# Kernel tuning notes

Measured on AMD Instinct MI355X. Metric: run time of the kernel, lower is better.

The kernel has to match this reference:

```python
import jax, jax.numpy as jnp
import numpy as np

# ---------- constants ----------
EPS = 1e-5
_rng = np.random.default_rng(0)
_P = _rng.normal(size=(8, 3))
_P /= np.linalg.norm(_P, axis=1, keepdims=True)

def _y2_np(p):
    x, y, z = p[:, 0], p[:, 1], p[:, 2]
    return np.stack([x * y, y * z, 3 * z * z - 1, x * z, x * x - y * y], axis=-1)

_A2 = np.linalg.pinv(_y2_np(_P)).astype(np.float32)  # [5,8]
P_C = jnp.asarray(_P.astype(np.float32))
A2_C = jnp.asarray(_A2)
NORM_CONST = np.float32(1.0 / np.sqrt(20.0))  # avg_num_neighbors ** -0.5
# res update (buffer zeros, not learnable): sigmoid(0)=0.5
_U = 0.5
C_OLD = np.float32(1.0 / np.sqrt(_U * _U + 1.0))
C_NEW = np.float32(_U * C_OLD)


def _y2(p):  # real l=2 monomial basis on unit vectors
    x, y, z = p[..., 0], p[..., 1], p[..., 2]
    return jnp.stack([x * y, y * z, 3.0 * z * z - 1.0, x * z, x * x - y * y], axis=-1)


def _frame(v):  # [E,3] -> R [E,3,3] with R @ v_hat = z
    n = v / jnp.linalg.norm(v, axis=-1, keepdims=True)
    z = jnp.array([0.0, 0.0, 1.0], v.dtype)
    xa = jnp.array([1.0, 0.0, 0.0], v.dtype)
    a = jnp.where(jnp.abs(n[:, 2:3]) < 0.99, z, xa)
    e1 = jnp.cross(a, n)
    e1 = e1 / jnp.linalg.norm(e1, axis=-1, keepdims=True)
    e2 = jnp.cross(n, e1)
    return jnp.stack([e1, e2, n], axis=1)


def _wigner_d2(R):  # [E,3,3] -> D2 [E,5,5] via sample-point fit
    pts = jnp.einsum('pj,eij->epi', P_C, R)  # R @ p_k, [E,8,3]
    M = _y2(pts)  # [E,8,5] = Y_P @ D^T
    Dt = jnp.einsum('ap,epb->eab', A2_C, M)  # [E,5,5]
    return jnp.swapaxes(Dt, 1, 2)


def _sln(x, w0, b0, w1, w2):  # separable equivariant layernorm, 32x0e+16x1e+8x2e
    s = x[:, :32]
    v1 = x[:, 32:80].reshape(-1, 16, 3)
    v2 = x[:, 80:120].reshape(-1, 8, 5)
    mu = jnp.mean(s, axis=-1, keepdims=True)
    var = jnp.mean((s - mu) ** 2, axis=-1, keepdims=True)
    s = (s - mu) * jax.lax.rsqrt(var + EPS) * w0 + b0
    var1 = jnp.mean(v1 ** 2, axis=(1, 2))  # degree-balanced component variance
    var2 = jnp.mean(v2 ** 2, axis=(1, 2))
    inv = jax.lax.rsqrt(0.5 * (var1 + var2) + EPS)[:, None, None]
    v1 = v1 * inv * w1[None, :, None]
    v2 = v2 * inv * w2[None, :, None]
    return jnp.concatenate([s, v1.reshape(-1, 48), v2.reshape(-1, 40)], axis=-1)


def _ir_linear(x, W0, b0, W1, W2):  # irreps-wise linear 32x0e+16x1e+8x2e -> same
    s = x[:, :32] @ (W0 / np.sqrt(32.0)) + b0
    v1 = jnp.einsum('eui,uv->evi', x[:, 32:80].reshape(-1, 16, 3), W1) / np.sqrt(16.0)
    v2 = jnp.einsum('eui,uv->evi', x[:, 80:120].reshape(-1, 8, 5), W2) / np.sqrt(8.0)
    return jnp.concatenate([s, v1.reshape(-1, 48), v2.reshape(-1, 40)], axis=-1)


def _so2(x_cat, R, D2f, D2b, w):  # SO2 linear with per-edge dynamic weights
    E = x_cat.shape[0]
    w0 = w[:, :8960].reshape(E, 112, 80)
    w1r = w[:, 8960:10112].reshape(E, 48, 24)
    w1i = w[:, 10112:11264].reshape(E, 48, 24)
    w2r = w[:, 11264:11392].reshape(E, 16, 8)
    w2i = w[:, 11392:11520].reshape(E, 16, 8)
    # split concatenated [in + hidden] blocks
    s = jnp.concatenate([x_cat[:, :32], x_cat[:, 120:152]], axis=-1)  # [E,64]
    v1 = jnp.concatenate([x_cat[:, 32:80].reshape(E, 16, 3),
                          x_cat[:, 152:200].reshape(E, 16, 3)], axis=1)  # [E,32,3]
    v2 = jnp.concatenate([x_cat[:, 80:120].reshape(E, 8, 5),
                          x_cat[:, 200:240].reshape(E, 16 // 2, 5)], axis=1)  # [E,16,5]
    # rotate into edge-aligned frame
    v1 = jnp.einsum('eij,euj->eui', R, v1)
    v2 = jnp.einsum('eij,euj->eui', D2f, v2)
    in0 = jnp.concatenate([s, v1[:, :, 1], v2[:, :, 2]], axis=-1)   # m=0, [E,112]
    inn1 = jnp.concatenate([v1[:, :, 0], v2[:, :, 1]], axis=-1)     # m=-1, [E,48]
    inp1 = jnp.concatenate([v1[:, :, 2], v2[:, :, 3]], axis=-1)     # m=+1
    inn2 = v2[:, :, 0]  # m=-2
    inp2 = v2[:, :, 4]  # m=+2
    out0 = jnp.einsum('ei,eio->eo', in0, w0) / np.sqrt(112.0)
    op1 = (jnp.einsum('ei,eio->eo', inp1, w1r) - jnp.einsum('ei,eio->eo', inn1, w1i)) / np.sqrt(48.0)
    on1 = (jnp.einsum('ei,eio->eo', inn1, w1r) + jnp.einsum('ei,eio->eo', inp1, w1i)) / np.sqrt(48.0)
    op2 = (jnp.einsum('ei,eio->eo', inp2, w2r) - jnp.einsum('ei,eio->eo', inn2, w2i)) / np.sqrt(16.0)
    on2 = (jnp.einsum('ei,eio->eo', inn2, w2r) + jnp.einsum('ei,eio->eo', inp2, w2i)) / np.sqrt(16.0)
    s_out = out0[:, :56]
    y1 = jnp.stack([on1[:, :16], out0[:, 56:72], op1[:, :16]], axis=-1)  # [E,16,3]
    y2o = jnp.stack([on2, on1[:, 16:24], out0[:, 72:80], op1[:, 16:24], op2], axis=-1)  # [E,8,5]
    # rotate back
    y1 = jnp.einsum('eij,euj->eui', jnp.swapaxes(R, 1, 2), y1)
    y2o = jnp.einsum('eij,euj->eui', D2b, y2o)
    return jnp.concatenate([s_out, y1.reshape(E, 48), y2o.reshape(E, 40)], axis=-1)  # [E,144]


def _gate(m):  # 32x0e scalars | 24x0e gates | 16x1e+8x2e gated
    s = jax.nn.silu(m[:, :32])
    g = jax.nn.sigmoid(m[:, 32:56])
    v1 = m[:, 56:104].reshape(-1, 16, 3) * g[:, :16, None]
    v2 = m[:, 104:144].reshape(-1, 8, 5) * g[:, 16:24, None]
    return jnp.concatenate([s, v1.reshape(-1, 48), v2.reshape(-1, 40)], axis=-1)


def _env(m, we):  # E3ElementLinear: per-mul elementwise weights
    s = m[:, :32] * we[:, :32]
    v1 = m[:, 32:80].reshape(-1, 16, 3) * we[:, 32:48, None]
    v2 = m[:, 80:120].reshape(-1, 8, 5) * we[:, 48:56, None]
    return jnp.concatenate([s, v1.reshape(-1, 48), v2.reshape(-1, 40)], axis=-1)


def setup_inputs() -> dict:
    key = jax.random.key(0)
    ks = jax.random.split(key, 16)
    N, E, L = 512, 10240, 128
    inp = {
        'latents': jax.random.normal(ks[0], (E, L), jnp.float32),
        'node_features': jax.random.normal(ks[1], (N, 120), jnp.float32),
        'hidden_features': jax.random.normal(ks[2], (E, 120), jnp.float32),
        'node_onehot': jnp.ones((N, 16), jnp.float32),
        'edge_vector': jax.random.normal(ks[3], (E, 3), jnp.float32),
        'W_tp': jax.random.normal(ks[4], (L, 11520), jnp.float32),
        'W_env': jax.random.normal(ks[5], (L, 56), jnp.float32),
        'sln_w0': jnp.ones((32,), jnp.float32),
        'sln_b0': jnp.zeros((32,), jnp.float32),
        'sln_w1': jnp.ones((16,), jnp.float32),
        'sln_w2': jnp.ones((8,), jnp.float32),
        'Wp0': jax.random.normal(ks[6], (32, 32), jnp.float32),
        'bp0': jnp.zeros((32,), jnp.float32),
        'Wp1': jax.random.normal(ks[7], (16, 16), jnp.float32),
        'Wp2': jax.random.normal(ks[8], (8, 8), jnp.float32),
        'Wr0': jax.random.normal(ks[9], (32, 32), jnp.float32),
        'br0': jnp.zeros((32,), jnp.float32),
        'Wr1': jax.random.normal(ks[10], (16, 16), jnp.float32),
        'Wr2': jax.random.normal(ks[11], (8, 8), jnp.float32),
        'atom_type': jax.random.randint(ks[12], (N,), 0, 10, jnp.int32),
        'edge_index': jax.random.randint(ks[13], (2, E), 0, N, jnp.int32),
        'active_edges': jnp.arange(E, dtype=jnp.int32),
    }
    return inp


def reference(latents, node_features, hidden_features, node_onehot, edge_vector,
              W_tp, W_env, sln_w0, sln_b0, sln_w1, sln_w2,
              Wp0, bp0, Wp1, Wp2, Wr0, br0, Wr1, Wr2,
              atom_type, edge_index, active_edges):
    n_nodes = node_features.shape[0]
    center = edge_index[0][active_edges]
    nf = _sln(node_features, sln_w0, sln_b0, sln_w1, sln_w2)
    x_cat = jnp.concatenate([nf[center], hidden_features], axis=-1)  # [E,240]
    v = edge_vector[active_edges]
    R = _frame(v)
    D2f = _wigner_d2(R)
    D2b = _wigner_d2(jnp.swapaxes(R, 1, 2))
    wdyn = latents @ (W_tp / np.sqrt(128.0))  # per-edge dynamic SO2 weights
    msg = _so2(x_cat, R, D2f, D2b, wdyn)
    msg = _gate(msg)
    msg = _ir_linear(msg, Wp0, bp0, Wp1, Wp2)
    wenv = latents[active_edges] @ (W_env / np.sqrt(128.0))
    weighted = _env(msg, wenv)
    new_nf = jax.ops.segment_sum(weighted, center, num_segments=n_nodes)
    new_nf = new_nf * NORM_CONST
    res = _ir_linear(node_features, Wr0, br0, Wr1, Wr2)
    return C_NEW * new_nf + C_OLD * res
```

## Files before the change

kernel.cpp:

```cpp
#include <hip/hip_runtime.h>
#include <math.h>

#define E_TOT   10240
#define N_NODES 512
#define NCOL    11520

typedef unsigned short ushort_t;
typedef unsigned int   uint_t;
typedef __bf16 bf16x8 __attribute__((ext_vector_type(8)));
typedef float  f32x4  __attribute__((ext_vector_type(4)));

constexpr float EPSF        = 1e-5f;
constexpr float INV_SQRT128 = 0.08838834764831845f;
constexpr float INV_SQRT112 = 0.09449111825230681f;
constexpr float INV_SQRT48  = 0.14433756729740643f;
constexpr float INV_SQRT32  = 0.17677669529663687f;
constexpr float INV_SQRT16  = 0.25f;
constexpr float INV_SQRT8   = 0.35355339059327373f;
constexpr float SC0 = INV_SQRT128 * INV_SQRT112;
constexpr float SC1 = INV_SQRT128 * INV_SQRT48;
constexpr float SC2 = INV_SQRT128 * INV_SQRT16;
constexpr float C_OLD_ = 0.8944271909999159f;
constexpr float C_NEW_ = 0.4472135954999579f;
constexpr float NORMC  = 0.22360679774997896f;
constexpr float OUTSC  = C_NEW_ * NORMC;

__device__ __forceinline__ ushort_t f2bf(float x) {
  uint_t u = __float_as_uint(x);
  u = (u + 0x7fffu + ((u >> 16) & 1u)) >> 16;
  return (ushort_t)u;
}

__device__ __forceinline__ void wigner5(const float q[9], float D[25]) {
  const float q0x=q[0],q0y=q[1],q0z=q[2];
  const float q1x=q[3],q1y=q[4],q1z=q[5];
  const float q2x=q[6],q2y=q[7],q2z=q[8];
  D[0]  = q0x*q1y + q1x*q0y;
  D[1]  = q0y*q1z + q1y*q0z;
  D[2]  = 0.5f*(q0z*q1z);
  D[3]  = q0x*q1z + q1x*q0z;
  D[4]  = 0.5f*(q0x*q1x - q0y*q1y);
  D[5]  = q1x*q2y + q2x*q1y;
  D[6]  = q1y*q2z + q2y*q1z;
  D[7]  = 0.5f*(q1z*q2z);
  D[8]  = q1x*q2z + q2x*q1z;
  D[9]  = 0.5f*(q1x*q2x - q1y*q2y);
  D[10] = 6.f*q2x*q2y;
  D[11] = 6.f*q2y*q2z;
  D[12] = 0.5f*(3.f*q2z*q2z - 1.f);
  D[13] = 6.f*q2x*q2z;
  D[14] = 1.5f*(q2x*q2x - q2y*q2y);
  D[15] = q0x*q2y + q2x*q0y;
  D[16] = q0y*q2z + q2y*q0z;
  D[17] = 0.5f*(q0z*q2z);
  D[18] = q0x*q2z + q2x*q0z;
  D[19] = 0.5f*(q0x*q2x - q0y*q2y);
  D[20] = 2.f*(q0x*q0y - q1x*q1y);
  D[21] = 2.f*(q0y*q0z - q1y*q1z);
  D[22] = 0.5f*(q0z*q0z - q1z*q1z);
  D[23] = 2.f*(q0x*q0z - q1x*q1z);
  D[24] = 0.5f*((q0x*q0x - q1x*q1x) - (q0y*q0y - q1y*q1y));
}

__global__ __launch_bounds__(256)
void kAB(const float* __restrict__ Wtp, const float* __restrict__ lat,
         const float* __restrict__ Wenv,
         const float* __restrict__ ndf, const float* __restrict__ hid,
         const float* __restrict__ evec,
         const int* __restrict__ eidx, const int* __restrict__ act,
         const float* __restrict__ w0, const float* __restrict__ b0,
         const float* __restrict__ w1, const float* __restrict__ w2,
         const float* __restrict__ Wr0, const float* __restrict__ br0,
         const float* __restrict__ Wr1, const float* __restrict__ Wr2,
         ushort_t* __restrict__ Wp,
         ushort_t* __restrict__ lath, ushort_t* __restrict__ latl,
         float* __restrict__ oa_g, float* __restrict__ WenvT,
         float* __restrict__ invT, float* __restrict__ Rm,
         float* __restrict__ D2bm, float* __restrict__ out) {
  __shared__ __align__(16) char smem[35584];
  const int bid = blockIdx.x;
  const int t = threadIdx.x;
  if (bid < 720) {
    float* Wl = (float*)smem;
    const int nt = bid;
    int col, tt;
    if (nt < 560)      { col = nt/112; tt = nt - col*112; }
    else if (nt < 608) { col = 5;  tt = nt-560; }
    else if (nt < 632) { col = 6;  tt = nt-608; }
    else if (nt < 680) { col = 7;  tt = nt-632; }
    else if (nt < 704) { col = 8;  tt = nt-680; }
    else if (nt < 712) { col = 9;  tt = nt-704; }
    else               { col = 10; tt = nt-712; }
    {
      const int m1 = t & 15, lp = t >> 4;
      int c; float sc;
      switch (col) {
        case 5:  c = 8960  + tt*24 + m1;                        sc = SC1; break;
        case 6:  c = 8960  + (2*tt + (m1>>3))*24 + 16 + (m1&7); sc = SC1; break;
        case 7:  c = 10112 + tt*24 + m1;                        sc = SC1; break;
        case 8:  c = 10112 + (2*tt + (m1>>3))*24 + 16 + (m1&7); sc = SC1; break;
        case 9:  c = 11264 + (2*tt + (m1>>3))*8 + (m1&7);       sc = SC2; break;
        case 10: c = 11392 + (2*tt + (m1>>3))*8 + (m1&7);       sc = SC2; break;
        default: c = tt*80 + col*16 + m1;                       sc = SC0; break;
      }
#pragma unroll
      for (int p = 0; p < 8; ++p) {
        int l = p*16 + lp;
        Wl[l*17 + m1] = Wtp[(size_t)l*NCOL + c] * sc;
      }
    }
    __syncthreads();
    const int kc = t >> 6, lane = t & 63;
    const int m = lane & 15, kg = lane >> 4;
    ushort_t hi[8], lo[8];
#pragma unroll
    for (int jj = 0; jj < 8; ++jj) {
      int l = kc*32 + kg*8 + jj;
      float w = Wl[l*17 + m];
      ushort_t h = f2bf(w);
      float hf = __uint_as_float(((uint_t)h) << 16);
      hi[jj] = h;
      lo[jj] = f2bf(w - hf);
    }
    size_t base = ((size_t)nt*8 + kc*2)*512 + (size_t)lane*8;
    *(uint4*)&Wp[base]       = *(const uint4*)hi;
    *(uint4*)&Wp[base + 512] = *(const uint4*)lo;
    return;
  }
  if (bid < 5840) {
    const int j = bid - 720;
    const int idx = j*256 + t;
    float x = lat[idx];
    ushort_t h = f2bf(x);
    float hf = __uint_as_float(((uint_t)h) << 16);
    lath[idx] = h;
    latl[idx] = f2bf(x - hf);
#pragma unroll
    for (int i = t; i < 288; i += 256) oa_g[(size_t)j*288 + i] = 0.f;
    if (j >= 4000 && j < 4028) {
      int q = (j-4000)*256 + t;
      int o = q >> 7, l = q & 127;
      WenvT[o*128 + l] = Wenv[l*56 + o];
    }
    return;
  }
  if (bid < 6160) {
    float (*xs)[240] = (float(*)[240])smem;
    float (*Rs)[9]   = (float(*)[9])(smem + 30720);
    float (*Dfs)[25] = (float(*)[25])(smem + 31872);
    float* muS  = (float*)(smem + 35072);
    float* isS  = (float*)(smem + 35200);
    float* invS = (float*)(smem + 35328);
    int*   ctrs = (int*)(smem + 35456);
    const int e0 = (bid - 5840)*32;
    if (t < 32) {
      const int e = e0 + t;
      const int ae = act[e];
      ctrs[t] = eidx[ae];
      float vx = evec[ae*3+0], vy = evec[ae*3+1], vz = evec[ae*3+2];
      float rn = rsqrtf(vx*vx + vy*vy + vz*vz);
      float nx = vx*rn, ny = vy*rn, nz = vz*rn;
      float e1x, e1y, e1z;
      if (fabsf(nz) < 0.99f) { e1x = -ny; e1y = nx;  e1z = 0.f; }
      else                   { e1x = 0.f; e1y = -nz; e1z = ny;  }
      float rl = rsqrtf(e1x*e1x + e1y*e1y + e1z*e1z);
      e1x *= rl; e1y *= rl; e1z *= rl;
      float e2x = ny*e1z - nz*e1y;
      float e2y = nz*e1x - nx*e1z;
      float e2z = nx*e1y - ny*e1x;
      float R[9] = {e1x,e1y,e1z, e2x,e2y,e2z, nx,ny,nz};
#pragma unroll
      for (int jj = 0; jj < 9; ++jj) { Rs[t][jj] = R[jj]; Rm[(size_t)e*9 + jj] = R[jj]; }
      float Df[25];
      wigner5(R, Df);
#pragma unroll
      for (int jj = 0; jj < 25; ++jj) Dfs[t][jj] = Df[jj];
      float Rt[9] = {R[0],R[3],R[6], R[1],R[4],R[7], R[2],R[5],R[8]};
      float Db[25];
      wigner5(Rt, Db);
#pragma unroll
      for (int jj = 0; jj < 25; ++jj) D2bm[(size_t)e*25 + jj] = Db[jj];
    }
    __syncthreads();
    for (int i = t; i < 32*120; i += 256) {
      int s = i/120, jj = i - s*120;
      xs[s][jj]     = ndf[(size_t)ctrs[s]*120 + jj];
      xs[s][120+jj] = hid[(size_t)(e0+s)*120 + jj];
    }
    __syncthreads();
    if (t < 32) {
      float sum = 0.f, sq = 0.f;
#pragma unroll
      for (int i = 0; i < 32; ++i) { float v = xs[t][i]; sum += v; sq += v*v; }
      float mu = sum*(1.f/32.f);
      float var = sq*(1.f/32.f) - mu*mu;
      float v1s = 0.f, v2s = 0.f;
#pragma unroll
      for (int i = 32; i < 80; ++i) { float v = xs[t][i]; v1s += v*v; }
#pragma unroll
      for (int i = 80; i < 120; ++i) { float v = xs[t][i]; v2s += v*v; }
      muS[t] = mu;
      isS[t] = rsqrtf(var + EPSF);
      invS[t] = rsqrtf(0.5f*(v1s*(1.f/48.f) + v2s*(1.f/40.f)) + EPSF);
    }
    __syncthreads();
    const int e = t & 31, rb = t >> 5;
    const float* X  = xs[e];
    const float* Rr = Rs[e];
    const float* Df = Dfs[e];
    const float mu = muS[e], istd = isS[e], inv = invS[e];
#pragma unroll
    for (int r = rb; r < 240; r += 8) {
      float val;
      if (r < 64) {
        if (r < 32) val = (X[r] - mu)*istd*w0[r] + b0[r];
        else        val = X[88 + r];
      } else if (r < 96) {
        int u = r - 64; int b; float fac;
        if (u < 16) { b = 32 + 3*u; fac = inv*w1[u]; } else { b = 152 + 3*(u-16); fac = 1.f; }
        val = (Rr[3]*X[b] + Rr[4]*X[b+1] + Rr[5]*X[b+2])*fac;
      } else if (r < 112) {
        int u = r - 96; int b; float fac;
        if (u < 8) { b = 80 + 5*u; fac = inv*w2[u]; } else { b = 200 + 5*(u-8); fac = 1.f; }
        val = (Df[10]*X[b] + Df[11]*X[b+1] + Df[12]*X[b+2] + Df[13]*X[b+3] + Df[14]*X[b+4])*fac;
      } else if (r < 160) {
        int u = r - 112;
        if (u < 32) {
          int b; float fac;
          if (u < 16) { b = 32 + 3*u; fac = inv*w1[u]; } else { b = 152 + 3*(u-16); fac = 1.f; }
          val = (Rr[0]*X[b] + Rr[1]*X[b+1] + Rr[2]*X[b+2])*fac;
        } else {
          int u2 = u - 32; int b; float fac;
          if (u2 < 8) { b = 80 + 5*u2; fac = inv*w2[u2]; } else { b = 200 + 5*(u2-8); fac = 1.f; }
          val = (Df[5]*X[b] + Df[6]*X[b+1] + Df[7]*X[b+2] + Df[8]*X[b+3] + Df[9]*X[b+4])*fac;
        }
      } else if (r < 208) {
        int u = r - 160;
        if (u < 32) {
          int b; float fac;
          if (u < 16) { b = 32 + 3*u; fac = inv*w1[u]; } else { b = 152 + 3*(u-16); fac = 1.f; }
          val = (Rr[6]*X[b] + Rr[7]*X[b+1] + Rr[8]*X[b+2])*fac;
        } else {
          int u2 = u - 32; int b; float fac;
          if (u2 < 8) { b = 80 + 5*u2; fac = inv*w2[u2]; } else { b = 200 + 5*(u2-8); fac = 1.f; }
          val = (Df[15]*X[b] + Df[16]*X[b+1] + Df[17]*X[b+2] + Df[18]*X[b+3] + Df[19]*X[b+4])*fac;
        }
      } else if (r < 224) {
        int u = r - 208; int b; float fac;
        if (u < 8) { b = 80 + 5*u; fac = inv*w2[u]; } else { b = 200 + 5*(u-8); fac = 1.f; }
        val = (Df[0]*X[b] + Df[1]*X[b+1] + Df[2]*X[b+2] + Df[3]*X[b+3] + Df[4]*X[b+4])*fac;
      } else {
        int u = r - 224; int b; float fac;
        if (u < 8) { b = 80 + 5*u; fac = inv*w2[u]; } else { b = 200 + 5*(u-8); fac = 1.f; }
        val = (Df[20]*X[b] + Df[21]*X[b+1] + Df[22]*X[b+2] + Df[23]*X[b+3] + Df[24]*X[b+4])*fac;
      }
      invT[(size_t)r*E_TOT + e0 + e] = val;
    }
    return;
  }
  {
    const int n = bid - 6160;
    if (t >= 120) return;
    const float* x = ndf + (size_t)n*120;
    float r;
    if (t < 32) {
      float s = 0.f;
#pragma unroll
      for (int i = 0; i < 32; ++i) s += x[i]*Wr0[i*32 + t];
      r = s*INV_SQRT32 + br0[t];
    } else if (t < 80) {
      int j = t - 32, v = j/3, cp = j - 3*v;
      float s = 0.f;
#pragma unroll
      for (int u = 0; u < 16; ++u) s += x[32 + u*3 + cp]*Wr1[u*16 + v];
      r = s*INV_SQRT16;
    } else {
      int j = t - 80, v = j/5, cp = j - 5*v;
      float s = 0.f;
#pragma unroll
      for (int u = 0; u < 8; ++u) s += x[80 + u*5 + cp]*Wr2[u*8 + v];
      r = s*INV_SQRT8;
    }
    out[(size_t)n*120 + t] = C_OLD_*r;
  }
}

struct Seg { int col, tt, mP, mN, sP, sN, segLen; float sg; bool PAIR, TWO; };
__device__ __forceinline__ void setp(Seg& s) {
  const int cf = s.col;
  if (cf < 5)       { s.segLen=112; s.mP=0;   s.mN=0;   s.sP=cf*16; s.sN=0;   s.sg=1.f;  s.PAIR=false; s.TWO=false; }
  else if (cf == 5) { s.segLen=48;  s.mP=160; s.mN=112; s.sP=80;  s.sN=104; s.sg=1.f;  s.PAIR=false; s.TWO=true; }
  else if (cf == 6) { s.segLen=24;  s.mP=160; s.mN=112; s.sP=96;  s.sN=120; s.sg=1.f;  s.PAIR=true;  s.TWO=true; }
  else if (cf == 7) { s.segLen=48;  s.mP=112; s.mN=160; s.sP=80;  s.sN=104; s.sg=-1.f; s.PAIR=false; s.TWO=true; }
  else if (cf == 8) { s.segLen=24;  s.mP=112; s.mN=160; s.sP=96;  s.sN=120; s.sg=-1.f; s.PAIR=true;  s.TWO=true; }
  else if (cf == 9) { s.segLen=8;   s.mP=224; s.mN=208; s.sP=128; s.sN=136; s.sg=1.f;  s.PAIR=true;  s.TWO=true; }
  else              { s.segLen=8;   s.mP=208; s.mN=224; s.sP=128; s.sN=136; s.sg=-1.f; s.PAIR=true;  s.TWO=true; }
}
__device__ __forceinline__ bool adv(Seg& s) {
  s.tt++;
  if (s.tt == s.segLen) { s.col++; s.tt = 0; setp(s); return true; }
  return false;
}

__global__ __launch_bounds__(256, 2)
void k3_gemm(const ushort_t* __restrict__ Wp,
             const ushort_t* __restrict__ lath,
             const ushort_t* __restrict__ latl,
             const float*  __restrict__ invT,
             float* __restrict__ oa_g) {
  __shared__ __align__(16) ushort_t abuf[2][8192];
  const int t = threadIdx.x;
  const int wave = t >> 6, lane = t & 63;
  const int le = lane & 15, g = lane >> 4, gh = g >> 1;
  const int fbase = blockIdx.y * 80;
  const int e0w = blockIdx.x*128 + wave*32;
  bf16x8 Bh[4][2], Bl[4][2];
#pragma unroll
  for (int kc = 0; kc < 4; ++kc)
#pragma unroll
    for (int n = 0; n < 2; ++n) {
      size_t off = (size_t)(e0w + n*16 + le)*128 + kc*32 + g*8;
      Bh[kc][n] = *(const bf16x8*)(lath + off);
      Bl[kc][n] = *(const bf16x8*)(latl + off);
    }
  Seg s;
  if (fbase < 560)      { s.col = fbase/112; s.tt = fbase - s.col*112; }
  else if (fbase < 608) { s.col = 5;  s.tt = fbase-560; }
  else if (fbase < 632) { s.col = 6;  s.tt = fbase-608; }
  else if (fbase < 680) { s.col = 7;  s.tt = fbase-632; }
  else if (fbase < 704) { s.col = 8;  s.tt = fbase-680; }
  else if (fbase < 712) { s.col = 9;  s.tt = fbase-704; }
  else                  { s.col = 10; s.tt = fbase-712; }
  setp(s);
  f32x4 aP0={0,0,0,0}, aP1={0,0,0,0}, aN0={0,0,0,0}, aN1={0,0,0,0};
  auto flushSeg = [&](const Seg& fs) {
#pragma unroll
    for (int r = 0; r < 4; ++r) {
      int mm = g*4 + r;
      int sp = fs.sP + (fs.PAIR ? (mm & 7) : mm);
      atomicAdd(&oa_g[(size_t)(e0w + le)*144 + sp], fs.sg*aP0[r]);
      atomicAdd(&oa_g[(size_t)(e0w + 16 + le)*144 + sp], fs.sg*aP1[r]);
      if (fs.TWO) {
        int sn = fs.sN + (fs.PAIR ? (mm & 7) : mm);
        atomicAdd(&oa_g[(size_t)(e0w + le)*144 + sn], aN0[r]);
        atomicAdd(&oa_g[(size_t)(e0w + 16 + le)*144 + sn], aN1[r]);
      }
    }
    aP0 = (f32x4){0,0,0,0}; aP1 = (f32x4){0,0,0,0};
    aN0 = (f32x4){0,0,0,0}; aN1 = (f32x4){0,0,0,0};
  };
#pragma unroll
  for (int qq = 0; qq < 4; ++qq) {
    uint4 v = *(const uint4*)(Wp + ((size_t)fbase*8 + wave*4 + qq)*512 + lane*8);
    *(uint4*)&abuf[0][(wave*4 + qq)*512 + lane*8] = v;
  }
  __syncthreads();
  for (int c = 0; c < 40; ++c) {
    const int cb = c & 1, nb = cb ^ 1;
    uint4 pre[4];
    const bool more = (c + 1) < 40;
    if (more) {
#pragma unroll
      for (int qq = 0; qq < 4; ++qq)
        pre[qq] = *(const uint4*)(Wp + ((size_t)(fbase + 2*(c+1))*8 + wave*4 + qq)*512 + lane*8);
    }
    Seg s1 = s;
    const bool cross0 = adv(s1);
    const int idx0 = s.PAIR  ? (2*s.tt  + gh) : s.tt;
    const int idx1 = s1.PAIR ? (2*s1.tt + gh) : s1.tt;
    float g0P0 = invT[(size_t)(s.mP + idx0)*E_TOT + e0w + le];
    float g0P1 = invT[(size_t)(s.mP + idx0)*E_TOT + e0w + 16 + le];
    float g1P0 = invT[(size_t)(s1.mP + idx1)*E_TOT + e0w + le];
    float g1P1 = invT[(size_t)(s1.mP + idx1)*E_TOT + e0w + 16 + le];
    float g0N0 = 0.f, g0N1 = 0.f, g1N0 = 0.f, g1N1 = 0.f;
    if (s.TWO) {
      g0N0 = invT[(size_t)(s.mN + idx0)*E_TOT + e0w + le];
      g0N1 = invT[(size_t)(s.mN + idx0)*E_TOT + e0w + 16 + le];
    }
    if (s1.TWO) {
      g1N0 = invT[(size_t)(s1.mN + idx1)*E_TOT + e0w + le];
      g1N1 = invT[(size_t)(s1.mN + idx1)*E_TOT + e0w + 16 + le];
    }
    {
      f32x4 dE0={0,0,0,0}, dO0={0,0,0,0}, dE1={0,0,0,0}, dO1={0,0,0,0};
#pragma unroll
      for (int kc = 0; kc < 2; ++kc) {
        bf16x8 Ah = *(const bf16x8*)&abuf[cb][(kc*2 + 0)*512 + lane*8];
        bf16x8 Al = *(const bf16x8*)&abuf[cb][(kc*2 + 1)*512 + lane*8];
        dE0 = __builtin_amdgcn_mfma_f32_16x16x32_bf16(Ah, Bh[kc][0], dE0, 0, 0, 0);
        dE1 = __builtin_amdgcn_mfma_f32_16x16x32_bf16(Ah, Bh[kc][1], dE1, 0, 0, 0);
        dE0 = __builtin_amdgcn_mfma_f32_16x16x32_bf16(Ah, Bl[kc][0], dE0, 0, 0, 0);
        dE1 = __builtin_amdgcn_mfma_f32_16x16x32_bf16(Ah, Bl[kc][1], dE1, 0, 0, 0);
        dE0 = __builtin_amdgcn_mfma_f32_16x16x32_bf16(Al, Bh[kc][0], dE0, 0, 0, 0);
        dE1 = __builtin_amdgcn_mfma_f32_16x16x32_bf16(Al, Bh[kc][1], dE1, 0, 0, 0);
      }
#pragma unroll
      for (int kc = 2; kc < 4; ++kc) {
        bf16x8 Ah = *(const bf16x8*)&abuf[cb][(kc*2 + 0)*512 + lane*8];
        bf16x8 Al = *(const bf16x8*)&abuf[cb][(kc*2 + 1)*512 + lane*8];
        dO0 = __builtin_amdgcn_mfma_f32_16x16x32_bf16(Ah, Bh[kc][0], dO0, 0, 0, 0);
        dO1 = __builtin_amdgcn_mfma_f32_16x16x32_bf16(Ah, Bh[kc][1], dO1, 0, 0, 0);
        dO0 = __builtin_amdgcn_mfma_f32_16x16x32_bf16(Ah, Bl[kc][0], dO0, 0, 0, 0);
        dO1 = __builtin_amdgcn_mfma_f32_16x16x32_bf16(Ah, Bl[kc][1], dO1, 0, 0, 0);
        dO0 = __builtin_amdgcn_mfma_f32_16x16x32_bf16(Al, Bh[kc][0], dO0, 0, 0, 0);
        dO1 = __builtin_amdgcn_mfma_f32_16x16x32_bf16(Al, Bh[kc][1], dO1, 0, 0, 0);
      }
      f32x4 d0 = dE0 + dO0, d1 = dE1 + dO1;
#pragma unroll
      for (int r = 0; r < 4; ++r) { aP0[r] += g0P0*d0[r]; aP1[r] += g0P1*d1[r]; }
      if (s.TWO) {
#pragma unroll
        for (int r = 0; r < 4; ++r) { aN0[r] += g0N0*d0[r]; aN1[r] += g0N1*d1[r]; }
      }
    }
    if (cross0) flushSeg(s);
    {
      f32x4 dE0={0,0,0,0}, dO0={0,0,0,0}, dE1={0,0,0,0}, dO1={0,0,0,0};
#pragma unroll
      for (int kc = 0; kc < 2; ++kc) {
        bf16x8 Ah = *(const bf16x8*)&abuf[cb][(8 + kc*2 + 0)*512 + lane*8];
        bf16x8 Al = *(const bf16x8*)&abuf[cb][(8 + kc*2 + 1)*512 + lane*8];
        dE0 = __builtin_amdgcn_mfma_f32_16x16x32_bf16(Ah, Bh[kc][0], dE0, 0, 0, 0);
        dE1 = __builtin_amdgcn_mfma_f32_16x16x32_bf16(Ah, Bh[kc][1], dE1, 0, 0, 0);
        dE0 = __builtin_amdgcn_mfma_f32_16x16x32_bf16(Ah, Bl[kc][0], dE0, 0, 0, 0);
        dE1 = __builtin_amdgcn_mfma_f32_16x16x32_bf16(Ah, Bl[kc][1], dE1, 0, 0, 0);
        dE0 = __builtin_amdgcn_mfma_f32_16x16x32_bf16(Al, Bh[kc][0], dE0, 0, 0, 0);
        dE1 = __builtin_amdgcn_mfma_f32_16x16x32_bf16(Al, Bh[kc][1], dE1, 0, 0, 0);
      }
#pragma unroll
      for (int kc = 2; kc < 4; ++kc) {
        bf16x8 Ah = *(const bf16x8*)&abuf[cb][(8 + kc*2 + 0)*512 + lane*8];
        bf16x8 Al = *(const bf16x8*)&abuf[cb][(8 + kc*2 + 1)*512 + lane*8];
        dO0 = __builtin_amdgcn_mfma_f32_16x16x32_bf16(Ah, Bh[kc][0], dO0, 0, 0, 0);
        dO1 = __builtin_amdgcn_mfma_f32_16x16x32_bf16(Ah, Bh[kc][1], dO1, 0, 0, 0);
        dO0 = __builtin_amdgcn_mfma_f32_16x16x32_bf16(Ah, Bl[kc][0], dO0, 0, 0, 0);
        dO1 = __builtin_amdgcn_mfma_f32_16x16x32_bf16(Ah, Bl[kc][1], dO1, 0, 0, 0);
        dO0 = __builtin_amdgcn_mfma_f32_16x16x32_bf16(Al, Bh[kc][0], dO0, 0, 0, 0);
        dO1 = __builtin_amdgcn_mfma_f32_16x16x32_bf16(Al, Bh[kc][1], dO1, 0, 0, 0);
      }
      f32x4 d0 = dE0 + dO0, d1 = dE1 + dO1;
#pragma unroll
      for (int r = 0; r < 4; ++r) { aP0[r] += g1P0*d0[r]; aP1[r] += g1P1*d1[r]; }
      if (s1.TWO) {
#pragma unroll
        for (int r = 0; r < 4; ++r) { aN0[r] += g1N0*d0[r]; aN1[r] += g1N1*d1[r]; }
      }
    }
    {
      Seg s2 = s1;
      const bool cross1 = adv(s2);
      if (cross1) flushSeg(s1);
      s = s2;
    }
    if (more) {
#pragma unroll
      for (int qq = 0; qq < 4; ++qq)
        *(uint4*)&abuf[nb][(wave*4 + qq)*512 + lane*8] = pre[qq];
    }
    __syncthreads();
  }
  if (s.tt > 0) flushSeg(s);
}

__global__ __launch_bounds__(256)
void k4_epi(const float* __restrict__ oa_g, const float* __restrict__ Rm,
            const float* __restrict__ D2bm,
            const float* __restrict__ lat, const float* __restrict__ WenvT,
            const int* __restrict__ eidx, const int* __restrict__ act,
            const float* __restrict__ Wp0, const float* __restrict__ bp0,
            const float* __restrict__ Wp1, const float* __restrict__ Wp2,
            float* __restrict__ out) {
  __shared__ float sc[4][200];
  const int wave = threadIdx.x >> 6, lane = threadIdx.x & 63;
  const int eg = blockIdx.x*4 + wave;
  const int ae = act[eg];
  const float* o_ = oa_g + (size_t)eg*144;
  if (lane < 56) {
    const float4* wv = (const float4*)(WenvT + lane*128);
    const float4* lv = (const float4*)(lat + (size_t)ae*128);
    float4 s4 = {0,0,0,0};
#pragma unroll
    for (int l4 = 0; l4 < 32; ++l4) {
      float4 a = lv[l4], b = wv[l4];
      s4.x += a.x*b.x; s4.y += a.y*b.y; s4.z += a.z*b.z; s4.w += a.w*b.w;
    }
    sc[wave][144 + lane] = (s4.x + s4.y + s4.z + s4.w) * INV_SQRT128;
    float v = o_[lane];
    sc[wave][lane] = (lane < 32) ? v/(1.f + expf(-v)) : 1.f/(1.f + expf(-v));
  }
  __syncthreads();
  const float* Rr = Rm + (size_t)eg*9;
  const float* Db = D2bm + (size_t)eg*25;
  if (lane < 48) {
    int u = lane/3, cc = lane - u*3;
    float yx = o_[104+u], yy = o_[56+u], yz = o_[80+u];
    float p = Rr[cc]*yx + Rr[3+cc]*yy + Rr[6+cc]*yz;
    sc[wave][56+lane] = p * sc[wave][32+u];
  }
  __syncthreads();
  if (lane < 40) {
    int u = lane/5, ii = lane - u*5;
    float y0 = o_[136+u], y1v = o_[120+u], y2v = o_[72+u], y3 = o_[96+u], y4 = o_[128+u];
    float p = Db[ii*5+0]*y0 + Db[ii*5+1]*y1v + Db[ii*5+2]*y2v + Db[ii*5+3]*y3 + Db[ii*5+4]*y4;
    sc[wave][104+lane] = p * sc[wave][48+u];
  }
  __syncthreads();
  const int ctr = eidx[ae];
  float* dst = out + (size_t)ctr*120;
  const float* we = &sc[wave][144];
#pragma unroll
  for (int rnd = 0; rnd < 2; ++rnd) {
    int jo = rnd*64 + lane;
    if (jo < 120) {
      float val;
      if (jo < 32) {
        float s = 0.f;
#pragma unroll
        for (int i2 = 0; i2 < 32; ++i2) s += sc[wave][i2]*Wp0[i2*32 + jo];
        val = (s*INV_SQRT32 + bp0[jo]) * we[jo];
      } else if (jo < 80) {
        int jj = jo-32, v = jj/3, cc = jj - v*3;
        float s = 0.f;
#pragma unroll
        for (int u = 0; u < 16; ++u) s += sc[wave][56 + u*3 + cc]*Wp1[u*16 + v];
        val = s*INV_SQRT16*we[32+v];
      } else {
        int jj = jo-80, v = jj/5, ii = jj - v*5;
        float s = 0.f;
#pragma unroll
        for (int u = 0; u < 8; ++u) s += sc[wave][104 + u*5 + ii]*Wp2[u*8 + v];
        val = s*INV_SQRT8*we[48+v];
      }
      atomicAdd(&dst[jo], OUTSC*val);
    }
  }
}

extern "C" void kernel_launch(void* const* d_in, const int* in_sizes, int n_in,
                              void* d_out, int out_size, void* d_ws, size_t ws_size,
                              hipStream_t stream) {
  const float* lat  = (const float*)d_in[0];
  const float* ndf  = (const float*)d_in[1];
  const float* hid  = (const float*)d_in[2];
  const float* evec = (const float*)d_in[4];
  const float* Wtp  = (const float*)d_in[5];
  const float* Wenv = (const float*)d_in[6];
  const float* w0   = (const float*)d_in[7];
  const float* b0   = (const float*)d_in[8];
  const float* w1   = (const float*)d_in[9];
  const float* w2   = (const float*)d_in[10];
  const float* Wp0  = (const float*)d_in[11];
  const float* bp0  = (const float*)d_in[12];
  const float* Wp1  = (const float*)d_in[13];
  const float* Wp2  = (const float*)d_in[14];
  const float* Wr0  = (const float*)d_in[15];
  const float* br0  = (const float*)d_in[16];
  const float* Wr1  = (const float*)d_in[17];
  const float* Wr2  = (const float*)d_in[18];
  const int*   eidx = (const int*)d_in[20];
  const int*   act  = (const int*)d_in[21];
  float* out = (float*)d_out;

  char* p = (char*)d_ws;
  float*    invT  = (float*)(p + 245760);
  float*    Rm    = (float*)(p + 10076160);
  float*    D2bm  = (float*)(p + 10444800);
  float*    oa_g  = (float*)(p + 14008320);
  ushort_t* lath  = (ushort_t*)(p + 19906560);
  ushort_t* latl  = (ushort_t*)(p + 22528000);
  ushort_t* Wpack = (ushort_t*)(p + 25149440);
  float*    WenvT = (float*)(p + 31047680);

  kAB<<<6672, 256, 0, stream>>>(Wtp, lat, Wenv, ndf, hid, evec, eidx, act,
                                w0, b0, w1, w2, Wr0, br0, Wr1, Wr2,
                                Wpack, lath, latl, oa_g, WenvT, invT, Rm, D2bm, out);
  k3_gemm<<<dim3(E_TOT/128, 9), 256, 0, stream>>>(Wpack, lath, latl, invT, oa_g);
  k4_epi<<<E_TOT/4, 256, 0, stream>>>(oa_g, Rm, D2bm, lat, WenvT, eidx, act,
                                      Wp0, bp0, Wp1, Wp2, out);
}
```

Measured before the change: 303.3 us.

## Precompute env weights in kAB, prefetch invT coefficients, raise GEMM occupancy

The per-edge latents@W_env projection moves out of the epilogue kernel into 40 new blocks of the first kernel. Each block stages W_env and a gathered latent chunk in shared memory and writes a [E,56] buffer that the epilogue then only reads. The GEMM kernel now software-prefetches the invT rotation coefficients for the next iteration into registers and raises the launch-bounds occupancy hint from 2 to 3. The costs are 56 accumulator registers per thread in the new blocks, more shared memory in kAB, and possible register spills in the GEMM under the tighter occupancy target.

```diff
diff --git a/kernel.cpp b/kernel.cpp
--- a/kernel.cpp
+++ b/kernel.cpp
@@ -74,10 +74,10 @@
          const float* __restrict__ Wr1, const float* __restrict__ Wr2,
          ushort_t* __restrict__ Wp,
          ushort_t* __restrict__ lath, ushort_t* __restrict__ latl,
-         float* __restrict__ oa_g, float* __restrict__ WenvT,
+         float* __restrict__ oa_g, float* __restrict__ wenvg,
          float* __restrict__ invT, float* __restrict__ Rm,
          float* __restrict__ D2bm, float* __restrict__ out) {
-  __shared__ __align__(16) char smem[35584];
+  __shared__ __align__(16) char smem[47104];
   const int bid = blockIdx.x;
   const int t = threadIdx.x;
   if (bid < 720) {
@@ -137,11 +137,6 @@
     latl[idx] = f2bf(x - hf);
 #pragma unroll
     for (int i = t; i < 288; i += 256) oa_g[(size_t)j*288 + i] = 0.f;
-    if (j >= 4000 && j < 4028) {
-      int q = (j-4000)*256 + t;
-      int o = q >> 7, l = q & 127;
-      WenvT[o*128 + l] = Wenv[l*56 + o];
-    }
     return;
   }
   if (bid < 6160) {
@@ -258,7 +253,7 @@
     }
     return;
   }
-  {
+  if (bid < 6672) {
     const int n = bid - 6160;
     if (t >= 120) return;
     const float* x = ndf + (size_t)n*120;
@@ -282,6 +277,36 @@
       r = s*INV_SQRT8;
     }
     out[(size_t)n*120 + t] = C_OLD_*r;
+    return;
+  }
+  {
+    float* Wl2  = (float*)smem;
+    float* latc = (float*)(smem + 28672);
+    int*   aes  = (int*)(smem + 46080);
+    const int e0 = (bid - 6672)*256;
+    for (int i = t; i < 128*56; i += 256) Wl2[i] = Wenv[i];
+    aes[t] = act[e0 + t];
+    float acc[56];
+#pragma unroll
+    for (int o = 0; o < 56; ++o) acc[o] = 0.f;
+    for (int lc = 0; lc < 8; ++lc) {
+      __syncthreads();
+      for (int i = t; i < 256*16; i += 256) {
+        int el = i >> 4, j = i & 15;
+        latc[el*17 + j] = lat[(size_t)aes[el]*128 + lc*16 + j];
+      }
+      __syncthreads();
+#pragma unroll
+      for (int j = 0; j < 16; ++j) {
+        float lv = latc[t*17 + j];
+        const float* wr = &Wl2[(lc*16 + j)*56];
+#pragma unroll
+        for (int o = 0; o < 56; ++o) acc[o] += lv * wr[o];
+      }
+    }
+    float* dst = wenvg + (size_t)(e0 + t)*56;
+#pragma unroll
+    for (int o = 0; o < 56; ++o) dst[o] = acc[o] * INV_SQRT128;
   }
 }
 
@@ -302,7 +327,7 @@
   return false;
 }
 
-__global__ __launch_bounds__(256, 2)
+__global__ __launch_bounds__(256, 3)
 void k3_gemm(const ushort_t* __restrict__ Wp,
              const ushort_t* __restrict__ lath,
              const ushort_t* __restrict__ latl,
@@ -332,6 +357,15 @@
   else if (fbase < 712) { s.col = 9;  s.tt = fbase-704; }
   else                  { s.col = 10; s.tt = fbase-712; }
   setp(s);
+  auto loadG = [&](const Seg& q, float& p0, float& p1, float& n0, float& n1) {
+    int idx = q.PAIR ? (2*q.tt + gh) : q.tt;
+    p0 = invT[(size_t)(q.mP + idx)*E_TOT + e0w + le];
+    p1 = invT[(size_t)(q.mP + idx)*E_TOT + e0w + 16 + le];
+    if (q.TWO) {
+      n0 = invT[(size_t)(q.mN + idx)*E_TOT + e0w + le];
+      n1 = invT[(size_t)(q.mN + idx)*E_TOT + e0w + 16 + le];
+    } else { n0 = 0.f; n1 = 0.f; }
+  };
   f32x4 aP0={0,0,0,0}, aP1={0,0,0,0}, aN0={0,0,0,0}, aN1={0,0,0,0};
   auto flushSeg = [&](const Seg& fs) {
 #pragma unroll
@@ -354,33 +388,29 @@
     uint4 v = *(const uint4*)(Wp + ((size_t)fbase*8 + wave*4 + qq)*512 + lane*8);
     *(uint4*)&abuf[0][(wave*4 + qq)*512 + lane*8] = v;
   }
+  float cP0[2], cP1[2], cN0[2], cN1[2];
+  {
+    Seg t0 = s; Seg t1 = s; adv(t1);
+    loadG(t0, cP0[0], cP1[0], cN0[0], cN1[0]);
+    loadG(t1, cP0[1], cP1[1], cN0[1], cN1[1]);
+  }
   __syncthreads();
   for (int c = 0; c < 40; ++c) {
     const int cb = c & 1, nb = cb ^ 1;
     uint4 pre[4];
     const bool more = (c + 1) < 40;
+    float nP0[2], nP1[2], nN0[2], nN1[2];
     if (more) {
 #pragma unroll
       for (int qq = 0; qq < 4; ++qq)
         pre[qq] = *(const uint4*)(Wp + ((size_t)(fbase + 2*(c+1))*8 + wave*4 + qq)*512 + lane*8);
+      Seg t0 = s; adv(t0); adv(t0);
+      Seg t1 = t0; adv(t1);
+      loadG(t0, nP0[0], nP1[0], nN0[0], nN1[0]);
+      loadG(t1, nP0[1], nP1[1], nN0[1], nN1[1]);
     }
     Seg s1 = s;
     const bool cross0 = adv(s1);
-    const int idx0 = s.PAIR  ? (2*s.tt  + gh) : s.tt;
-    const int idx1 = s1.PAIR ? (2*s1.tt + gh) : s1.tt;
-    float g0P0 = invT[(size_t)(s.mP + idx0)*E_TOT + e0w + le];
-    float g0P1 = invT[(size_t)(s.mP + idx0)*E_TOT + e0w + 16 + le];
-    float g1P0 = invT[(size_t)(s1.mP + idx1)*E_TOT + e0w + le];
-    float g1P1 = invT[(size_t)(s1.mP + idx1)*E_TOT + e0w + 16 + le];
-    float g0N0 = 0.f, g0N1 = 0.f, g1N0 = 0.f, g1N1 = 0.f;
-    if (s.TWO) {
-      g0N0 = invT[(size_t)(s.mN + idx0)*E_TOT + e0w + le];
-      g0N1 = invT[(size_t)(s.mN + idx0)*E_TOT + e0w + 16 + le];
-    }
-    if (s1.TWO) {
-      g1N0 = invT[(size_t)(s1.mN + idx1)*E_TOT + e0w + le];
-      g1N1 = invT[(size_t)(s1.mN + idx1)*E_TOT + e0w + 16 + le];
-    }
     {
       f32x4 dE0={0,0,0,0}, dO0={0,0,0,0}, dE1={0,0,0,0}, dO1={0,0,0,0};
 #pragma unroll
@@ -407,10 +437,10 @@
       }
       f32x4 d0 = dE0 + dO0, d1 = dE1 + dO1;
 #pragma unroll
-      for (int r = 0; r < 4; ++r) { aP0[r] += g0P0*d0[r]; aP1[r] += g0P1*d1[r]; }
+      for (int r = 0; r < 4; ++r) { aP0[r] += cP0[0]*d0[r]; aP1[r] += cP1[0]*d1[r]; }
       if (s.TWO) {
 #pragma unroll
-        for (int r = 0; r < 4; ++r) { aN0[r] += g0N0*d0[r]; aN1[r] += g0N1*d1[r]; }
+        for (int r = 0; r < 4; ++r) { aN0[r] += cN0[0]*d0[r]; aN1[r] += cN1[0]*d1[r]; }
       }
     }
     if (cross0) flushSeg(s);
@@ -440,10 +470,10 @@
       }
       f32x4 d0 = dE0 + dO0, d1 = dE1 + dO1;
 #pragma unroll
-      for (int r = 0; r < 4; ++r) { aP0[r] += g1P0*d0[r]; aP1[r] += g1P1*d1[r]; }
+      for (int r = 0; r < 4; ++r) { aP0[r] += cP0[1]*d0[r]; aP1[r] += cP1[1]*d1[r]; }
       if (s1.TWO) {
 #pragma unroll
-        for (int r = 0; r < 4; ++r) { aN0[r] += g1N0*d0[r]; aN1[r] += g1N1*d1[r]; }
+        for (int r = 0; r < 4; ++r) { aN0[r] += cN0[1]*d0[r]; aN1[r] += cN1[1]*d1[r]; }
       }
     }
     {
@@ -452,6 +482,11 @@
       if (cross1) flushSeg(s1);
       s = s2;
     }
+#pragma unroll
+    for (int q2 = 0; q2 < 2; ++q2) {
+      cP0[q2] = nP0[q2]; cP1[q2] = nP1[q2];
+      cN0[q2] = nN0[q2]; cN1[q2] = nN1[q2];
+    }
     if (more) {
 #pragma unroll
       for (int qq = 0; qq < 4; ++qq)
@@ -464,8 +499,7 @@
 
 __global__ __launch_bounds__(256)
 void k4_epi(const float* __restrict__ oa_g, const float* __restrict__ Rm,
-            const float* __restrict__ D2bm,
-            const float* __restrict__ lat, const float* __restrict__ WenvT,
+            const float* __restrict__ D2bm, const float* __restrict__ wenvg,
             const int* __restrict__ eidx, const int* __restrict__ act,
             const float* __restrict__ Wp0, const float* __restrict__ bp0,
             const float* __restrict__ Wp1, const float* __restrict__ Wp2,
@@ -476,15 +510,7 @@
   const int ae = act[eg];
   const float* o_ = oa_g + (size_t)eg*144;
   if (lane < 56) {
-    const float4* wv = (const float4*)(WenvT + lane*128);
-    const float4* lv = (const float4*)(lat + (size_t)ae*128);
-    float4 s4 = {0,0,0,0};
-#pragma unroll
-    for (int l4 = 0; l4 < 32; ++l4) {
-      float4 a = lv[l4], b = wv[l4];
-      s4.x += a.x*b.x; s4.y += a.y*b.y; s4.z += a.z*b.z; s4.w += a.w*b.w;
-    }
-    sc[wave][144 + lane] = (s4.x + s4.y + s4.z + s4.w) * INV_SQRT128;
+    sc[wave][144 + lane] = wenvg[(size_t)eg*56 + lane];
     float v = o_[lane];
     sc[wave][lane] = (lane < 32) ? v/(1.f + expf(-v)) : 1.f/(1.f + expf(-v));
   }
@@ -565,16 +591,16 @@
   float*    invT  = (float*)(p + 245760);
   float*    Rm    = (float*)(p + 10076160);
   float*    D2bm  = (float*)(p + 10444800);
+  float*    wenvg = (float*)(p + 11468800);
   float*    oa_g  = (float*)(p + 14008320);
   ushort_t* lath  = (ushort_t*)(p + 19906560);
   ushort_t* latl  = (ushort_t*)(p + 22528000);
   ushort_t* Wpack = (ushort_t*)(p + 25149440);
-  float*    WenvT = (float*)(p + 31047680);
-
-  kAB<<<6672, 256, 0, stream>>>(Wtp, lat, Wenv, ndf, hid, evec, eidx, act,
+
+  kAB<<<6712, 256, 0, stream>>>(Wtp, lat, Wenv, ndf, hid, evec, eidx, act,
                                 w0, b0, w1, w2, Wr0, br0, Wr1, Wr2,
-                                Wpack, lath, latl, oa_g, WenvT, invT, Rm, D2bm, out);
+                                Wpack, lath, latl, oa_g, wenvg, invT, Rm, D2bm, out);
   k3_gemm<<<dim3(E_TOT/128, 9), 256, 0, stream>>>(Wpack, lath, latl, invT, oa_g);
-  k4_epi<<<E_TOT/4, 256, 0, stream>>>(oa_g, Rm, D2bm, lat, WenvT, eidx, act,
+  k4_epi<<<E_TOT/4, 256, 0, stream>>>(oa_g, Rm, D2bm, wenvg, eidx, act,
                                       Wp0, bp0, Wp1, Wp2, out);
 }
```

New measurement: 284.2 us. 1.07x faster.
